# Kernel tuning notes

Measured on AMD Instinct MI355X. Metric: run time of the kernel, lower is better.

The kernel has to match this reference:

```python
import jax, jax.numpy as jnp
import numpy as np

B, SQ, SK, HID, NH = 4, 2048, 2048, 1024, 16
HD = HID // NH  # head dim = 64


def setup_inputs() -> dict:
    key = jax.random.key(0)
    ks = jax.random.split(key, 8)
    s = 1.0 / np.sqrt(HID)
    return {
        "hidden_states": jax.random.normal(ks[0], (B, SQ, HID), jnp.float32),
        "context": jax.random.normal(ks[1], (B, SK, HID), jnp.float32),
        "Wq": jax.random.normal(ks[2], (HID, HID), jnp.float32) * s,
        "bq": jnp.zeros((HID,), jnp.float32),
        "Wk": jax.random.normal(ks[3], (HID, HID), jnp.float32) * s,
        "bk": jnp.zeros((HID,), jnp.float32),
        "Wv": jax.random.normal(ks[4], (HID, HID), jnp.float32) * s,
        "bv": jnp.zeros((HID,), jnp.float32),
    }


def _heads(x):
    # [B, S, HID] -> [B, NH, S, HD]
    b, s, _ = x.shape
    return x.reshape(b, s, NH, HD).transpose(0, 2, 1, 3)


def reference(hidden_states, context, Wq, bq, Wk, bk, Wv, bv):
    q = _heads(hidden_states @ Wq + bq)   # [B,NH,SQ,HD]
    k = _heads(context @ Wk + bk)         # [B,NH,SK,HD]
    v = _heads(context @ Wv + bv)         # [B,NH,SK,HD]
    scores = jnp.einsum("bhqd,bhkd->bhqk", q, k) / jnp.sqrt(jnp.float32(HD))
    probs = jax.nn.softmax(scores, axis=-1)  # dropout p=0 (eval) -> identity
    ctx = jnp.einsum("bhqk,bhkd->bhqd", probs, v)
    return ctx.transpose(0, 2, 1, 3).reshape(hidden_states.shape[0], -1, NH * HD)
```

## Files before the change

### kernel.cpp

```cpp
#include <hip/hip_runtime.h>
#include <hip/hip_bf16.h>
#include <math.h>

#define DI __device__ __forceinline__

typedef unsigned short u16;
typedef unsigned int u32;
typedef __bf16 bf16x8 __attribute__((ext_vector_type(8)));
typedef float f32x4 __attribute__((ext_vector_type(4)));
typedef float f32x16 __attribute__((ext_vector_type(16)));
typedef u16 u16x4 __attribute__((ext_vector_type(4)));
typedef u16 u16x8 __attribute__((ext_vector_type(8)));
typedef u32 u32x4 __attribute__((ext_vector_type(4)));

DI void gload16(const void* g, void* l) {
  __builtin_amdgcn_global_load_lds(
      (__attribute__((address_space(1))) void*)(g),
      (__attribute__((address_space(3))) void*)(l), 16, 0, 0);
}

DI u16 f2bf(float f) {
  u32 u = __builtin_bit_cast(u32, f);
  return (u16)((u + 0x7fffu + ((u >> 16) & 1u)) >> 16);
}

DI u32 cvtpk(float lo, float hi_) {
  u32 r; asm("v_cvt_pk_bf16_f32 %0, %1, %2" : "=v"(r) : "v"(lo), "v"(hi_)); return r;
}

#define MFMA16(a, b, c) __builtin_amdgcn_mfma_f32_16x16x32_bf16(a, b, c, 0, 0, 0)
#define MFMA32(a, b, c) __builtin_amdgcn_mfma_f32_32x32x16_bf16(a, b, c, 0, 0, 0)

__global__ __launch_bounds__(256) void k_convert(const float* __restrict__ a,
                                                 const float* __restrict__ b,
                                                 u16* __restrict__ oa, u16* __restrict__ ob) {
  const float* src = blockIdx.y ? b : a;
  u16* dst = blockIdx.y ? ob : oa;
  const int n4 = (4 * 2048 * 1024) / 4;
  for (int i = blockIdx.x * blockDim.x + threadIdx.x; i < n4; i += gridDim.x * blockDim.x) {
    float4 v = ((const float4*)src)[i];
    u16x4 o;
    o[0] = f2bf(v.x); o[1] = f2bf(v.y); o[2] = f2bf(v.z); o[3] = f2bf(v.w);
    *(u16x4*)(dst + 4 * (size_t)i) = o;
  }
}

__global__ __launch_bounds__(256) void k_transW(const float* __restrict__ Wq,
                                                const float* __restrict__ Wk,
                                                const float* __restrict__ Wv,
                                                u16* __restrict__ Wt) {
  __shared__ u16 tile[64][72];
  const float* W = blockIdx.z == 0 ? Wq : (blockIdx.z == 1 ? Wk : Wv);
  u16* out = Wt + (size_t)blockIdx.z * (1024 * 1024);
  int k0 = blockIdx.x * 64, n0 = blockIdx.y * 64;
  int t = threadIdx.x, r = t >> 2, c0 = (t & 3) * 16;
  const float4* src = (const float4*)(W + (size_t)(k0 + r) * 1024 + n0 + c0);
#pragma unroll
  for (int i = 0; i < 4; ++i) {
    float4 v = src[i];
    tile[r][c0 + 4 * i + 0] = f2bf(v.x); tile[r][c0 + 4 * i + 1] = f2bf(v.y);
    tile[r][c0 + 4 * i + 2] = f2bf(v.z); tile[r][c0 + 4 * i + 3] = f2bf(v.w);
  }
  __syncthreads();
  u16x8 o0, o1;
#pragma unroll
  for (int i = 0; i < 8; ++i) { o0[i] = tile[c0 + i][r]; o1[i] = tile[c0 + 8 + i][r]; }
  u16* dst = out + (size_t)(n0 + r) * 1024 + k0 + c0;
  *(u16x8*)dst = o0; *(u16x8*)(dst + 8) = o1;
}

__global__ __launch_bounds__(256) void k_gemm(const u16* __restrict__ A,
                                              const u16* __restrict__ Bt,
                                              const float* __restrict__ bias,
                                              u16* __restrict__ C, float scale) {
  __shared__ __attribute__((aligned(16))) u16 As[2][128 * 32];
  __shared__ __attribute__((aligned(16))) u16 Bs[2][128 * 32];
  const int t = threadIdx.x, w = t >> 6, l = t & 63, g = l >> 4, lid = l & 15;
  const int wr = w >> 1, wc = w & 1;
  const int m0 = blockIdx.x * 128, n0 = blockIdx.y * 128;
  f32x4 acc[4][4] = {};

  auto stage = [&](int buf, int kt) {
    for (int i = 0; i < 2; ++i) {
      int slot = i * 256 + t;
      int row = slot >> 2, c = slot & 3;
      gload16(A + (size_t)(m0 + row) * 1024 + kt * 32 + ((c ^ (row & 3)) << 3),
              &As[buf][slot << 3]);
      gload16(Bt + (size_t)(n0 + row) * 1024 + kt * 32 + ((c ^ (row & 3)) << 3),
              &Bs[buf][slot << 3]);
    }
  };

  stage(0, 0);
  __syncthreads();
  int cur = 0;
  for (int kt = 0; kt < 32; ++kt) {
    if (kt + 1 < 32) stage(cur ^ 1, kt + 1);
    bf16x8 af[4], bfr[4];
#pragma unroll
    for (int mi = 0; mi < 4; ++mi) {
      int row = wr * 64 + mi * 16 + lid;
      af[mi] = *(const bf16x8*)&As[cur][(row << 5) + ((g ^ (row & 3)) << 3)];
    }
#pragma unroll
    for (int ni = 0; ni < 4; ++ni) {
      int row = wc * 64 + ni * 16 + lid;
      bfr[ni] = *(const bf16x8*)&Bs[cur][(row << 5) + ((g ^ (row & 3)) << 3)];
    }
#pragma unroll
    for (int mi = 0; mi < 4; ++mi)
#pragma unroll
      for (int ni = 0; ni < 4; ++ni)
        acc[mi][ni] = MFMA16(af[mi], bfr[ni], acc[mi][ni]);
    __syncthreads();
    cur ^= 1;
  }
#pragma unroll
  for (int ni = 0; ni < 4; ++ni) {
    int n = n0 + wc * 64 + ni * 16 + lid;
    float bb = bias[n];
    int h = n >> 6, d = n & 63;
#pragma unroll
    for (int mi = 0; mi < 4; ++mi) {
      int mb = m0 + wr * 64 + mi * 16 + g * 4;
#pragma unroll
      for (int j = 0; j < 4; ++j) {
        int m = mb + j;
        int b = m >> 11, s = m & 2047;
        C[((size_t)(b * 16 + h) << 17) + ((size_t)s << 6) + d] =
            f2bf((acc[mi][ni][j] + bb) * scale);
      }
    }
  }
}

__global__ __launch_bounds__(256) void k_transV(const u16* __restrict__ V,
                                                u16* __restrict__ Vt) {
  __shared__ u16 tile[64][72];
  int h = blockIdx.y, s0 = blockIdx.x * 64;
  int t = threadIdx.x, r = t >> 2, c0 = (t & 3) * 16;
  const u16x8* src = (const u16x8*)(V + (size_t)h * 131072 + (size_t)(s0 + r) * 64 + c0);
  u16x8 a = src[0], b = src[1];
#pragma unroll
  for (int i = 0; i < 8; ++i) { tile[r][c0 + i] = a[i]; tile[r][c0 + 8 + i] = b[i]; }
  __syncthreads();
  u16x8 o0, o1;
#pragma unroll
  for (int i = 0; i < 8; ++i) { o0[i] = tile[c0 + i][r]; o1[i] = tile[c0 + 8 + i][r]; }
  u16* dst = Vt + (size_t)h * 131072 + (size_t)r * 2048 + s0 + c0;
  *(u16x8*)dst = o0; *(u16x8*)(dst + 8) = o1;
}

__global__ __launch_bounds__(256) void k_attn(const u16* __restrict__ Q,
                                              const u16* __restrict__ K,
                                              const u16* __restrict__ Vt,
                                              float* __restrict__ Out) {
  __shared__ __attribute__((aligned(16))) u16 smem[16384];
  u16* Ks = smem;
  u16* Vs = smem + 8192;
  const int t = threadIdx.x, w = t >> 6, l = t & 63;
  const int ql = l & 31, hi = l >> 5;
  const int head = blockIdx.y, q0 = blockIdx.x * 128;
  const size_t hoff = (size_t)head * 131072;
  const u16* Qh = Q + hoff + (size_t)q0 * 64;
  const u16* Kh = K + hoff;
  const u16* Vh = Vt + hoff;

  for (int i = 0; i < 4; ++i) {
    int slot = i * 256 + t, row = slot >> 3, c = slot & 7;
    gload16(Qh + (size_t)row * 64 + ((c ^ (row & 7)) << 3), &smem[slot << 3]);
  }
  __syncthreads();
  bf16x8 qf[4];
  const int qrow = w * 32 + ql;
#pragma unroll
  for (int dt = 0; dt < 4; ++dt) {
    int ch = dt * 2 + hi;
    qf[dt] = *(const bf16x8*)&smem[(qrow << 6) + ((ch ^ (qrow & 7)) << 3)];
  }
  __syncthreads();

  auto stageKV = [&](int buf, int kv0) {
    for (int i = 0; i < 2; ++i) {
      int slot = i * 256 + t, row = slot >> 3, c = slot & 7;
      gload16(Kh + (size_t)(kv0 + row) * 64 + ((c ^ (row & 7)) << 3),
              &Ks[buf * 4096 + (slot << 3)]);
      gload16(Vh + (size_t)row * 2048 + kv0 + ((c ^ (row & 7)) << 3),
              &Vs[buf * 4096 + (slot << 3)]);
    }
  };

  f32x16 ot0 = {}, ot1 = {};
  float m = -1e30f, lsum = 0.f;

  stageKV(0, 0);
  __syncthreads();
  int cur = 0;
  for (int tt = 0; tt < 32; ++tt) {
    if (tt + 1 < 32) stageKV(cur ^ 1, (tt + 1) * 64);
    const u16* Kb = &Ks[cur * 4096];
    const u16* Vb = &Vs[cur * 4096];
    f32x16 st0 = {}, st1 = {};
#pragma unroll
    for (int dt = 0; dt < 4; ++dt) {
      int ch = dt * 2 + hi;
      {
        int row = ql;
        bf16x8 kf = *(const bf16x8*)&Kb[(row << 6) + ((ch ^ (row & 7)) << 3)];
        st0 = MFMA32(kf, qf[dt], st0);
      }
      {
        int row = 32 + ql;
        bf16x8 kf = *(const bf16x8*)&Kb[(row << 6) + ((ch ^ (row & 7)) << 3)];
        st1 = MFMA32(kf, qf[dt], st1);
      }
    }
    float rm = st0[0];
#pragma unroll
    for (int r = 1; r < 16; ++r) rm = fmaxf(rm, st0[r]);
#pragma unroll
    for (int r = 0; r < 16; ++r) rm = fmaxf(rm, st1[r]);
    rm = fmaxf(rm, __shfl_xor(rm, 32, 64));
    if (!__all(rm <= m + 8.f)) {
      float mn = fmaxf(m, rm);
      float sc = exp2f(m - mn);
      m = mn;
#pragma unroll
      for (int r = 0; r < 16; ++r) { ot0[r] *= sc; ot1[r] *= sc; }
      lsum *= sc;
    }
    float rs = 0.f;
#pragma unroll
    for (int r = 0; r < 16; ++r) { st0[r] = exp2f(st0[r] - m); rs += st0[r]; }
#pragma unroll
    for (int r = 0; r < 16; ++r) { st1[r] = exp2f(st1[r] - m); rs += st1[r]; }
    rs += __shfl_xor(rs, 32, 64);
    lsum += rs;
#define PVCHUNK(sp, rb, c)                                                    \
    do {                                                                      \
      u32 a0 = cvtpk(sp[rb + 0], sp[rb + 1]);                                 \
      u32 a1 = cvtpk(sp[rb + 2], sp[rb + 3]);                                 \
      u32 b0 = cvtpk(sp[rb + 4], sp[rb + 5]);                                 \
      u32 b1 = cvtpk(sp[rb + 6], sp[rb + 7]);                                 \
      u32 pa0 = __shfl_xor(a0, 32, 64);                                       \
      u32 pa1 = __shfl_xor(a1, 32, 64);                                       \
      u32 pb0 = __shfl_xor(b0, 32, 64);                                       \
      u32 pb1 = __shfl_xor(b1, 32, 64);                                       \
      u32x4 pw;                                                               \
      pw[0] = hi ? pb0 : a0;                                  \
      pw[1] = hi ? pb1 : a1;                                  \
      pw[2] = hi ? b0 : pa0;                                  \
      pw[3] = hi ? b1 : pa1;                                  \
      bf16x8 pf = __builtin_bit_cast(bf16x8, pw);                             \
      {                                                                       \
        int row = ql, ch = (c) * 2 + hi;                                      \
        bf16x8 vf = *(const bf16x8*)&Vb[(row << 6) + ((ch ^ (row & 7)) << 3)];\
        ot0 = MFMA32(vf, pf, ot0);                                            \
      }                                                                       \
      {                                                                       \
        int row = 32 + ql, ch = (c) * 2 + hi;                                 \
        bf16x8 vf = *(const bf16x8*)&Vb[(row << 6) + ((ch ^ (row & 7)) << 3)];\
        ot1 = MFMA32(vf, pf, ot1);                                            \
      }                                                                       \
    } while (0)
    PVCHUNK(st0, 0, 0);
    PVCHUNK(st0, 8, 1);
    PVCHUNK(st1, 0, 2);
    PVCHUNK(st1, 8, 3);
#undef PVCHUNK
    __syncthreads();
    cur ^= 1;
  }
  const int b = head >> 4, h = head & 15;
  const int qg = q0 + w * 32 + ql;
  float inv = 1.f / lsum;
  float* op = Out + ((size_t)b * 2048 + qg) * 1024 + h * 64;
#pragma unroll
  for (int rq = 0; rq < 4; ++rq) {
    f32x4 v0, v1;
#pragma unroll
    for (int j = 0; j < 4; ++j) {
      v0[j] = ot0[rq * 4 + j] * inv;
      v1[j] = ot1[rq * 4 + j] * inv;
    }
    *(f32x4*)(op + rq * 8 + 4 * hi) = v0;
    *(f32x4*)(op + 32 + rq * 8 + 4 * hi) = v1;
  }
}

extern "C" void kernel_launch(void* const* d_in, const int* in_sizes, int n_in,
                              void* d_out, int out_size, void* d_ws, size_t ws_size,
                              hipStream_t stream) {
  const float* hs  = (const float*)d_in[0];
  const float* ctx = (const float*)d_in[1];
  const float* Wq  = (const float*)d_in[2];
  const float* bq  = (const float*)d_in[3];
  const float* Wk  = (const float*)d_in[4];
  const float* bk  = (const float*)d_in[5];
  const float* Wv  = (const float*)d_in[6];
  const float* bv  = (const float*)d_in[7];
  float* out = (float*)d_out;

  u16* hsb  = (u16*)d_ws;
  u16* ctxb = hsb + 8388608;
  u16* Wt   = ctxb + 8388608;
  u16* Qb   = Wt + 3 * 1048576;
  u16* Kb   = Qb + 8388608;
  u16* Vtb  = Kb + 8388608;
  u16* Vb   = hsb;

  const float CC = 0.18033688011112042f;

  k_convert<<<dim3(2048, 2), 256, 0, stream>>>(hs, ctx, hsb, ctxb);
  k_transW<<<dim3(16, 16, 3), 256, 0, stream>>>(Wq, Wk, Wv, Wt);
  k_gemm<<<dim3(64, 8), 256, 0, stream>>>(hsb, Wt, bq, Qb, CC);
  k_gemm<<<dim3(64, 8), 256, 0, stream>>>(ctxb, Wt + 1048576, bk, Kb, 1.0f);
  k_gemm<<<dim3(64, 8), 256, 0, stream>>>(ctxb, Wt + 2097152, bv, Vb, 1.0f);
  k_transV<<<dim3(32, 64), 256, 0, stream>>>(Vb, Vtb);
  k_attn<<<dim3(16, 64), 256, 0, stream>>>(Qb, Kb, Vtb, out);
}
```

Before: 356.0 us.

## Write V transposed from GEMM epilogue and tree-reduce softmax max/sum

The V projection GEMM now writes its output directly in the transposed [head, d, seq] layout with 4-wide vector stores. This removes the separate k_transV kernel launch and its extra read and write of V. Separately, the attention kernel's per-row max and sum reductions become pairwise tree reductions instead of serial chains, which shortens dependency latency. The transposed stores are strided by 2048 elements per d, so each lane's 8-byte write may coalesce worse than the original row-major layout.

```diff
diff --git a/kernel.cpp b/kernel.cpp
--- a/kernel.cpp
+++ b/kernel.cpp
@@ -72,7 +72,7 @@
 __global__ __launch_bounds__(256) void k_gemm(const u16* __restrict__ A,
                                               const u16* __restrict__ Bt,
                                               const float* __restrict__ bias,
-                                              u16* __restrict__ C, float scale) {
+                                              u16* __restrict__ C, float scale, int vt) {
   __shared__ __attribute__((aligned(16))) u16 As[2][128 * 32];
   __shared__ __attribute__((aligned(16))) u16 Bs[2][128 * 32];
   const int t = threadIdx.x, w = t >> 6, l = t & 63, g = l >> 4, lid = l & 15;
@@ -123,32 +123,23 @@
 #pragma unroll
     for (int mi = 0; mi < 4; ++mi) {
       int mb = m0 + wr * 64 + mi * 16 + g * 4;
-#pragma unroll
-      for (int j = 0; j < 4; ++j) {
-        int m = mb + j;
-        int b = m >> 11, s = m & 2047;
-        C[((size_t)(b * 16 + h) << 17) + ((size_t)s << 6) + d] =
-            f2bf((acc[mi][ni][j] + bb) * scale);
+      if (vt) {
+        int b = mb >> 11, sl = mb & 2047;
+        u16x4 o;
+#pragma unroll
+        for (int j = 0; j < 4; ++j) o[j] = f2bf((acc[mi][ni][j] + bb) * scale);
+        *(u16x4*)&C[(size_t)(b * 16 + h) * 131072 + (size_t)d * 2048 + sl] = o;
+      } else {
+#pragma unroll
+        for (int j = 0; j < 4; ++j) {
+          int m = mb + j;
+          int b = m >> 11, s = m & 2047;
+          C[((size_t)(b * 16 + h) << 17) + ((size_t)s << 6) + d] =
+              f2bf((acc[mi][ni][j] + bb) * scale);
+        }
       }
     }
   }
-}
-
-__global__ __launch_bounds__(256) void k_transV(const u16* __restrict__ V,
-                                                u16* __restrict__ Vt) {
-  __shared__ u16 tile[64][72];
-  int h = blockIdx.y, s0 = blockIdx.x * 64;
-  int t = threadIdx.x, r = t >> 2, c0 = (t & 3) * 16;
-  const u16x8* src = (const u16x8*)(V + (size_t)h * 131072 + (size_t)(s0 + r) * 64 + c0);
-  u16x8 a = src[0], b = src[1];
-#pragma unroll
-  for (int i = 0; i < 8; ++i) { tile[r][c0 + i] = a[i]; tile[r][c0 + 8 + i] = b[i]; }
-  __syncthreads();
-  u16x8 o0, o1;
-#pragma unroll
-  for (int i = 0; i < 8; ++i) { o0[i] = tile[c0 + i][r]; o1[i] = tile[c0 + 8 + i][r]; }
-  u16* dst = Vt + (size_t)h * 131072 + (size_t)r * 2048 + s0 + c0;
-  *(u16x8*)dst = o0; *(u16x8*)(dst + 8) = o1;
 }
 
 __global__ __launch_bounds__(256) void k_attn(const u16* __restrict__ Q,
@@ -215,11 +206,14 @@
         st1 = MFMA32(kf, qf[dt], st1);
       }
     }
-    float rm = st0[0];
-#pragma unroll
-    for (int r = 1; r < 16; ++r) rm = fmaxf(rm, st0[r]);
-#pragma unroll
-    for (int r = 0; r < 16; ++r) rm = fmaxf(rm, st1[r]);
+    float mx[16];
+#pragma unroll
+    for (int r = 0; r < 16; ++r) mx[r] = fmaxf(st0[r], st1[r]);
+#pragma unroll
+    for (int s = 8; s; s >>= 1)
+#pragma unroll
+      for (int r = 0; r < s; ++r) mx[r] = fmaxf(mx[r], mx[r + s]);
+    float rm = mx[0];
     rm = fmaxf(rm, __shfl_xor(rm, 32, 64));
     if (!__all(rm <= m + 8.f)) {
       float mn = fmaxf(m, rm);
@@ -229,11 +223,18 @@
       for (int r = 0; r < 16; ++r) { ot0[r] *= sc; ot1[r] *= sc; }
       lsum *= sc;
     }
-    float rs = 0.f;
-#pragma unroll
-    for (int r = 0; r < 16; ++r) { st0[r] = exp2f(st0[r] - m); rs += st0[r]; }
-#pragma unroll
-    for (int r = 0; r < 16; ++r) { st1[r] = exp2f(st1[r] - m); rs += st1[r]; }
+#pragma unroll
+    for (int r = 0; r < 16; ++r) st0[r] = exp2f(st0[r] - m);
+#pragma unroll
+    for (int r = 0; r < 16; ++r) st1[r] = exp2f(st1[r] - m);
+    float sm[16];
+#pragma unroll
+    for (int r = 0; r < 16; ++r) sm[r] = st0[r] + st1[r];
+#pragma unroll
+    for (int s = 8; s; s >>= 1)
+#pragma unroll
+      for (int r = 0; r < s; ++r) sm[r] += sm[r + s];
+    float rs = sm[0];
     rs += __shfl_xor(rs, 32, 64);
     lsum += rs;
 #define PVCHUNK(sp, rb, c)                                                    \
@@ -307,15 +308,13 @@
   u16* Qb   = Wt + 3 * 1048576;
   u16* Kb   = Qb + 8388608;
   u16* Vtb  = Kb + 8388608;
-  u16* Vb   = hsb;
 
   const float CC = 0.18033688011112042f;
 
   k_convert<<<dim3(2048, 2), 256, 0, stream>>>(hs, ctx, hsb, ctxb);
   k_transW<<<dim3(16, 16, 3), 256, 0, stream>>>(Wq, Wk, Wv, Wt);
-  k_gemm<<<dim3(64, 8), 256, 0, stream>>>(hsb, Wt, bq, Qb, CC);
-  k_gemm<<<dim3(64, 8), 256, 0, stream>>>(ctxb, Wt + 1048576, bk, Kb, 1.0f);
-  k_gemm<<<dim3(64, 8), 256, 0, stream>>>(ctxb, Wt + 2097152, bv, Vb, 1.0f);
-  k_transV<<<dim3(32, 64), 256, 0, stream>>>(Vb, Vtb);
+  k_gemm<<<dim3(64, 8), 256, 0, stream>>>(hsb, Wt, bq, Qb, CC, 0);
+  k_gemm<<<dim3(64, 8), 256, 0, stream>>>(ctxb, Wt + 1048576, bk, Kb, 1.0f, 0);
+  k_gemm<<<dim3(64, 8), 256, 0, stream>>>(ctxb, Wt + 2097152, bv, Vtb, 1.0f, 1);
   k_attn<<<dim3(16, 64), 256, 0, stream>>>(Qb, Kb, Vtb, out);
 }
```

After: 351.6 us. About the same (-1.2%).
